# Performance work log

Hardware: AMD Instinct MI355X
Metric: run time of the kernel (lower is better)

## Reference

```python
import jax, jax.numpy as jnp
import numpy as np

N_EMB = 384
BLOCK = 128

def setup_inputs() -> dict:
    key = jax.random.key(0)
    k1, k2, k3, k4 = jax.random.split(key, 4)
    B, T, hs = 1024, 128, 64
    x = jax.random.normal(k1, (B, T, N_EMB), dtype=jnp.float32)
    Wk = jax.random.normal(k2, (hs, N_EMB), dtype=jnp.float32) * (N_EMB ** -0.5)
    Wq = jax.random.normal(k3, (hs, N_EMB), dtype=jnp.float32) * (N_EMB ** -0.5)
    Wv = jax.random.normal(k4, (hs, N_EMB), dtype=jnp.float32) * (N_EMB ** -0.5)
    return {"x": x, "Wk": Wk, "Wq": Wq, "Wv": Wv}

def reference(x, Wk, Wq, Wv):
    B, T, C = x.shape
    # nn.Linear(n_emb, head_size, bias=False): y = x @ W.T
    k = jnp.einsum('btc,hc->bth', x, Wk)  # [B,T,hs]
    q = jnp.einsum('btc,hc->bth', x, Wq)
    v = jnp.einsum('btc,hc->bth', x, Wv)
    # NOTE: source scales by C**-0.5 where C = n_emb (384), not head_size
    w = jnp.einsum('bth,bsh->bts', q, k) * (C ** -0.5)  # [B,T,T]
    causal = jnp.tril(jnp.ones((T, T), dtype=bool))
    w = jnp.where(causal, w, -jnp.inf)
    w = jax.nn.softmax(w, axis=-1)
    # dropout is identity in eval mode
    out = jnp.einsum('bts,bsh->bth', w, v)  # [B,T,hs]
    return out
```

## Files before the change

kernel.cpp:

```cpp
#include <hip/hip_runtime.h>

typedef __bf16 bf16_t;
typedef __attribute__((ext_vector_type(8))) __bf16 bf16x8;
typedef __attribute__((ext_vector_type(4))) float floatx4;

#define MFMA16(a, b, c) __builtin_amdgcn_mfma_f32_16x16x32_bf16((a), (b), (c), 0, 0, 0)

constexpr int TT = 128;
constexpr int CD = 384;
constexpr int HS = 64;
constexpr int W_ELEMS = HS * CD;

constexpr int QK_STR = 72;
constexpr int VT_STR = 136;
constexpr int QS_OFF = 0;
constexpr int KS_OFF = TT * QK_STR;
constexpr int VT_OFF = 2 * TT * QK_STR;
constexpr int PS_OFF = 0;
constexpr int SMEM_N = 2 * TT * QK_STR + HS * VT_STR;

__global__ void wconv_kernel(const float* __restrict__ wq, const float* __restrict__ wk,
                             const float* __restrict__ wv, bf16_t* __restrict__ out) {
    int i = blockIdx.x * 256 + threadIdx.x;
    if (i < W_ELEMS)            out[i] = (bf16_t)wq[i];
    else if (i < 2 * W_ELEMS)   out[i] = (bf16_t)wk[i - W_ELEMS];
    else if (i < 3 * W_ELEMS)   out[i] = (bf16_t)wv[i - 2 * W_ELEMS];
}

__launch_bounds__(256, 2)
__global__ void attn_kernel(const float* __restrict__ x, const bf16_t* __restrict__ wc,
                            float* __restrict__ out) {
    __shared__ bf16_t smem[SMEM_N];
    const int b    = blockIdx.x;
    const int lane = threadIdx.x & 63;
    const int w    = threadIdx.x >> 6;
    const int l15  = lane & 15;
    const int g    = lane >> 4;
    const float* xb = x + (size_t)b * TT * CD;

    floatx4 accq[2][4], acck[2][4], accv[2][4];
#pragma unroll
    for (int mt = 0; mt < 2; ++mt)
#pragma unroll
        for (int nt = 0; nt < 4; ++nt) {
            accq[mt][nt] = (floatx4)0.0f;
            acck[mt][nt] = (floatx4)0.0f;
            accv[mt][nt] = (floatx4)0.0f;
        }

    for (int kk = 0; kk < CD; kk += 32) {
        const int c = kk + 8 * g;
        bf16x8 a[2];
#pragma unroll
        for (int mt = 0; mt < 2; ++mt) {
            const int row = 32 * w + 16 * mt + l15;
            const float* p = xb + row * CD + c;
            float4 f0 = *(const float4*)p;
            float4 f1 = *(const float4*)(p + 4);
            bf16x8 t;
            t[0] = (bf16_t)f0.x; t[1] = (bf16_t)f0.y; t[2] = (bf16_t)f0.z; t[3] = (bf16_t)f0.w;
            t[4] = (bf16_t)f1.x; t[5] = (bf16_t)f1.y; t[6] = (bf16_t)f1.z; t[7] = (bf16_t)f1.w;
            a[mt] = t;
        }
#pragma unroll
        for (int nt = 0; nt < 4; ++nt) {
            const int h = 16 * nt + l15;
            bf16x8 bq = *(const bf16x8*)(wc + 0 * W_ELEMS + h * CD + c);
            bf16x8 bk = *(const bf16x8*)(wc + 1 * W_ELEMS + h * CD + c);
            bf16x8 bv = *(const bf16x8*)(wc + 2 * W_ELEMS + h * CD + c);
            accq[0][nt] = MFMA16(a[0], bq, accq[0][nt]);
            accq[1][nt] = MFMA16(a[1], bq, accq[1][nt]);
            acck[0][nt] = MFMA16(a[0], bk, acck[0][nt]);
            acck[1][nt] = MFMA16(a[1], bk, acck[1][nt]);
            accv[0][nt] = MFMA16(a[0], bv, accv[0][nt]);
            accv[1][nt] = MFMA16(a[1], bv, accv[1][nt]);
        }
    }

#pragma unroll
    for (int mt = 0; mt < 2; ++mt)
#pragma unroll
        for (int nt = 0; nt < 4; ++nt) {
            const int t0 = 32 * w + 16 * mt + 4 * g;
            const int h  = 16 * nt + l15;
#pragma unroll
            for (int r = 0; r < 4; ++r) {
                smem[QS_OFF + (t0 + r) * QK_STR + h] = (bf16_t)accq[mt][nt][r];
                smem[KS_OFF + (t0 + r) * QK_STR + h] = (bf16_t)acck[mt][nt][r];
                smem[VT_OFF + h * VT_STR + t0 + r]   = (bf16_t)accv[mt][nt][r];
            }
        }
    __syncthreads();

    floatx4 sacc[2][8];
#pragma unroll
    for (int mt = 0; mt < 2; ++mt)
#pragma unroll
        for (int nt = 0; nt < 8; ++nt) sacc[mt][nt] = (floatx4)0.0f;

#pragma unroll
    for (int kt = 0; kt < 2; ++kt) {
        const int hh = 32 * kt + 8 * g;
        bf16x8 aq[2];
        aq[0] = *(const bf16x8*)(smem + QS_OFF + (32 * w + l15) * QK_STR + hh);
        aq[1] = *(const bf16x8*)(smem + QS_OFF + (32 * w + 16 + l15) * QK_STR + hh);
#pragma unroll
        for (int nt = 0; nt < 8; ++nt) {
            if (16 * nt <= 32 * w + 31) {
                bf16x8 bk = *(const bf16x8*)(smem + KS_OFF + (16 * nt + l15) * QK_STR + hh);
                if (16 * nt <= 32 * w + 15) sacc[0][nt] = MFMA16(aq[0], bk, sacc[0][nt]);
                sacc[1][nt] = MFMA16(aq[1], bk, sacc[1][nt]);
            }
        }
    }
    __syncthreads();

    const float scale = 0.05103103630798287f;
#pragma unroll
    for (int mt = 0; mt < 2; ++mt) {
#pragma unroll
        for (int r = 0; r < 4; ++r) {
            const int t = 32 * w + 16 * mt + 4 * g + r;
            float vals[8];
            float vmax = -__builtin_inff();
#pragma unroll
            for (int nt = 0; nt < 8; ++nt) {
                const int s = 16 * nt + l15;
                float v = (s <= t) ? sacc[mt][nt][r] * scale : -__builtin_inff();
                vals[nt] = v;
                vmax = fmaxf(vmax, v);
            }
            vmax = fmaxf(vmax, __shfl_xor(vmax, 1));
            vmax = fmaxf(vmax, __shfl_xor(vmax, 2));
            vmax = fmaxf(vmax, __shfl_xor(vmax, 4));
            vmax = fmaxf(vmax, __shfl_xor(vmax, 8));
            float sum = 0.0f;
#pragma unroll
            for (int nt = 0; nt < 8; ++nt) {
                float e = __expf(vals[nt] - vmax);
                vals[nt] = e;
                sum += e;
            }
            sum += __shfl_xor(sum, 1);
            sum += __shfl_xor(sum, 2);
            sum += __shfl_xor(sum, 4);
            sum += __shfl_xor(sum, 8);
            const float inv = 1.0f / sum;
#pragma unroll
            for (int nt = 0; nt < 8; ++nt)
                smem[PS_OFF + t * VT_STR + 16 * nt + l15] = (bf16_t)(vals[nt] * inv);
        }
    }

    floatx4 oacc[2][4];
#pragma unroll
    for (int mt = 0; mt < 2; ++mt)
#pragma unroll
        for (int nt = 0; nt < 4; ++nt) oacc[mt][nt] = (floatx4)0.0f;

    for (int st = 0; st <= w; ++st) {
        const int ss = 32 * st + 8 * g;
        bf16x8 ap[2];
        ap[0] = *(const bf16x8*)(smem + PS_OFF + (32 * w + l15) * VT_STR + ss);
        ap[1] = *(const bf16x8*)(smem + PS_OFF + (32 * w + 16 + l15) * VT_STR + ss);
#pragma unroll
        for (int nt = 0; nt < 4; ++nt) {
            bf16x8 bv = *(const bf16x8*)(smem + VT_OFF + (16 * nt + l15) * VT_STR + ss);
            oacc[0][nt] = MFMA16(ap[0], bv, oacc[0][nt]);
            oacc[1][nt] = MFMA16(ap[1], bv, oacc[1][nt]);
        }
    }

    float* ob = out + (size_t)b * TT * HS;
#pragma unroll
    for (int mt = 0; mt < 2; ++mt)
#pragma unroll
        for (int nt = 0; nt < 4; ++nt) {
            const int t0 = 32 * w + 16 * mt + 4 * g;
            const int h  = 16 * nt + l15;
#pragma unroll
            for (int r = 0; r < 4; ++r)
                ob[(t0 + r) * HS + h] = oacc[mt][nt][r];
        }
}

extern "C" void kernel_launch(void* const* d_in, const int* in_sizes, int n_in,
                              void* d_out, int out_size, void* d_ws, size_t ws_size,
                              hipStream_t stream) {
    const float* x  = (const float*)d_in[0];
    const float* wk = (const float*)d_in[1];
    const float* wq = (const float*)d_in[2];
    const float* wv = (const float*)d_in[3];
    bf16_t* wc = (bf16_t*)d_ws;
    float* out = (float*)d_out;

    wconv_kernel<<<(3 * W_ELEMS + 255) / 256, 256, 0, stream>>>(wq, wk, wv, wc);
    attn_kernel<<<1024, 256, 0, stream>>>(x, wc, out);
}
```

Before: 342.2 us.

## Split fused attention into separate QKV projection and attention kernels via global workspace

```diff
diff --git a/kernel.cpp b/kernel.cpp
--- a/kernel.cpp
+++ b/kernel.cpp
@@ -1,6 +1,7 @@
 #include <hip/hip_runtime.h>
 
 typedef __bf16 bf16_t;
+typedef __attribute__((ext_vector_type(4))) __bf16 bf16x4;
 typedef __attribute__((ext_vector_type(8))) __bf16 bf16x8;
 typedef __attribute__((ext_vector_type(4))) float floatx4;
 
@@ -9,15 +10,10 @@
 constexpr int TT = 128;
 constexpr int CD = 384;
 constexpr int HS = 64;
+constexpr int BB = 1024;
 constexpr int W_ELEMS = HS * CD;
-
-constexpr int QK_STR = 72;
-constexpr int VT_STR = 136;
-constexpr int QS_OFF = 0;
-constexpr int KS_OFF = TT * QK_STR;
-constexpr int VT_OFF = 2 * TT * QK_STR;
-constexpr int PS_OFF = 0;
-constexpr int SMEM_N = 2 * TT * QK_STR + HS * VT_STR;
+constexpr size_t QKV_ELEMS = (size_t)BB * TT * HS;
+constexpr int PS_STR = 136;
 
 __global__ void wconv_kernel(const float* __restrict__ wq, const float* __restrict__ wk,
                              const float* __restrict__ wv, bf16_t* __restrict__ out) {
@@ -27,97 +23,94 @@
     else if (i < 3 * W_ELEMS)   out[i] = (bf16_t)wv[i - 2 * W_ELEMS];
 }
 
-__launch_bounds__(256, 2)
-__global__ void attn_kernel(const float* __restrict__ x, const bf16_t* __restrict__ wc,
-                            float* __restrict__ out) {
-    __shared__ bf16_t smem[SMEM_N];
-    const int b    = blockIdx.x;
+__launch_bounds__(256, 4)
+__global__ void qkv_kernel(const float* __restrict__ x, const bf16_t* __restrict__ wc,
+                           bf16_t* __restrict__ q, bf16_t* __restrict__ k,
+                           bf16_t* __restrict__ vt) {
     const int lane = threadIdx.x & 63;
     const int w    = threadIdx.x >> 6;
     const int l15  = lane & 15;
     const int g    = lane >> 4;
-    const float* xb = x + (size_t)b * TT * CD;
+    const int row0 = blockIdx.x * 64 + w * 16;
+    const float* xr = x + (size_t)(row0 + l15) * CD;
 
-    floatx4 accq[2][4], acck[2][4], accv[2][4];
+    floatx4 accq[4], acck[4], accv[4];
 #pragma unroll
-    for (int mt = 0; mt < 2; ++mt)
-#pragma unroll
-        for (int nt = 0; nt < 4; ++nt) {
-            accq[mt][nt] = (floatx4)0.0f;
-            acck[mt][nt] = (floatx4)0.0f;
-            accv[mt][nt] = (floatx4)0.0f;
-        }
+    for (int nt = 0; nt < 4; ++nt) {
+        accq[nt] = (floatx4)0.0f;
+        acck[nt] = (floatx4)0.0f;
+        accv[nt] = (floatx4)0.0f;
+    }
 
     for (int kk = 0; kk < CD; kk += 32) {
         const int c = kk + 8 * g;
-        bf16x8 a[2];
-#pragma unroll
-        for (int mt = 0; mt < 2; ++mt) {
-            const int row = 32 * w + 16 * mt + l15;
-            const float* p = xb + row * CD + c;
-            float4 f0 = *(const float4*)p;
-            float4 f1 = *(const float4*)(p + 4);
-            bf16x8 t;
-            t[0] = (bf16_t)f0.x; t[1] = (bf16_t)f0.y; t[2] = (bf16_t)f0.z; t[3] = (bf16_t)f0.w;
-            t[4] = (bf16_t)f1.x; t[5] = (bf16_t)f1.y; t[6] = (bf16_t)f1.z; t[7] = (bf16_t)f1.w;
-            a[mt] = t;
-        }
+        float4 f0 = *(const float4*)(xr + c);
+        float4 f1 = *(const float4*)(xr + c + 4);
+        bf16x8 a;
+        a[0] = (bf16_t)f0.x; a[1] = (bf16_t)f0.y; a[2] = (bf16_t)f0.z; a[3] = (bf16_t)f0.w;
+        a[4] = (bf16_t)f1.x; a[5] = (bf16_t)f1.y; a[6] = (bf16_t)f1.z; a[7] = (bf16_t)f1.w;
 #pragma unroll
         for (int nt = 0; nt < 4; ++nt) {
             const int h = 16 * nt + l15;
             bf16x8 bq = *(const bf16x8*)(wc + 0 * W_ELEMS + h * CD + c);
             bf16x8 bk = *(const bf16x8*)(wc + 1 * W_ELEMS + h * CD + c);
             bf16x8 bv = *(const bf16x8*)(wc + 2 * W_ELEMS + h * CD + c);
-            accq[0][nt] = MFMA16(a[0], bq, accq[0][nt]);
-            accq[1][nt] = MFMA16(a[1], bq, accq[1][nt]);
-            acck[0][nt] = MFMA16(a[0], bk, acck[0][nt]);
-            acck[1][nt] = MFMA16(a[1], bk, acck[1][nt]);
-            accv[0][nt] = MFMA16(a[0], bv, accv[0][nt]);
-            accv[1][nt] = MFMA16(a[1], bv, accv[1][nt]);
+            accq[nt] = MFMA16(a, bq, accq[nt]);
+            acck[nt] = MFMA16(a, bk, acck[nt]);
+            accv[nt] = MFMA16(a, bv, accv[nt]);
         }
     }
 
+    const int b  = row0 >> 7;
+    const int tl = (row0 & 127) + 4 * g;
+#pragma unroll
+    for (int nt = 0; nt < 4; ++nt) {
+        const int h = 16 * nt + l15;
+#pragma unroll
+        for (int r = 0; r < 4; ++r) {
+            const size_t rowg = (size_t)(row0 + 4 * g + r);
+            q[rowg * HS + h] = (bf16_t)accq[nt][r];
+            k[rowg * HS + h] = (bf16_t)acck[nt][r];
+        }
+        bf16x4 pv;
+        pv[0] = (bf16_t)accv[nt][0]; pv[1] = (bf16_t)accv[nt][1];
+        pv[2] = (bf16_t)accv[nt][2]; pv[3] = (bf16_t)accv[nt][3];
+        *(bf16x4*)(vt + (size_t)b * HS * TT + (size_t)h * TT + tl) = pv;
+    }
+}
+
+__launch_bounds__(256, 4)
+__global__ void attn2_kernel(const bf16_t* __restrict__ q, const bf16_t* __restrict__ k,
+                             const bf16_t* __restrict__ vt, float* __restrict__ out) {
+    __shared__ __align__(16) bf16_t pbuf[TT * PS_STR];
+    const int b    = blockIdx.x;
+    const int lane = threadIdx.x & 63;
+    const int w    = threadIdx.x >> 6;
+    const int l15  = lane & 15;
+    const int g    = lane >> 4;
+    const size_t qb = (size_t)b * TT * HS;
+    const float scale = 0.05103103630798287f;
+
+    bf16x8 aq[2][2];
 #pragma unroll
     for (int mt = 0; mt < 2; ++mt)
 #pragma unroll
-        for (int nt = 0; nt < 4; ++nt) {
-            const int t0 = 32 * w + 16 * mt + 4 * g;
-            const int h  = 16 * nt + l15;
+        for (int kt = 0; kt < 2; ++kt)
+            aq[mt][kt] = *(const bf16x8*)(q + qb + (size_t)(32 * w + 16 * mt + l15) * HS + 32 * kt + 8 * g);
+
 #pragma unroll
-            for (int r = 0; r < 4; ++r) {
-                smem[QS_OFF + (t0 + r) * QK_STR + h] = (bf16_t)accq[mt][nt][r];
-                smem[KS_OFF + (t0 + r) * QK_STR + h] = (bf16_t)acck[mt][nt][r];
-                smem[VT_OFF + h * VT_STR + t0 + r]   = (bf16_t)accv[mt][nt][r];
+    for (int mt = 0; mt < 2; ++mt) {
+        floatx4 sacc[8];
+#pragma unroll
+        for (int nt = 0; nt < 8; ++nt) sacc[nt] = (floatx4)0.0f;
+        const int ntmax = 2 * w + mt;
+#pragma unroll
+        for (int kt = 0; kt < 2; ++kt) {
+            for (int nt = 0; nt <= ntmax; ++nt) {
+                bf16x8 bk = *(const bf16x8*)(k + qb + (size_t)(16 * nt + l15) * HS + 32 * kt + 8 * g);
+                sacc[nt] = MFMA16(aq[mt][kt], bk, sacc[nt]);
             }
         }
-    __syncthreads();
-
-    floatx4 sacc[2][8];
-#pragma unroll
-    for (int mt = 0; mt < 2; ++mt)
-#pragma unroll
-        for (int nt = 0; nt < 8; ++nt) sacc[mt][nt] = (floatx4)0.0f;
-
-#pragma unroll
-    for (int kt = 0; kt < 2; ++kt) {
-        const int hh = 32 * kt + 8 * g;
-        bf16x8 aq[2];
-        aq[0] = *(const bf16x8*)(smem + QS_OFF + (32 * w + l15) * QK_STR + hh);
-        aq[1] = *(const bf16x8*)(smem + QS_OFF + (32 * w + 16 + l15) * QK_STR + hh);
-#pragma unroll
-        for (int nt = 0; nt < 8; ++nt) {
-            if (16 * nt <= 32 * w + 31) {
-                bf16x8 bk = *(const bf16x8*)(smem + KS_OFF + (16 * nt + l15) * QK_STR + hh);
-                if (16 * nt <= 32 * w + 15) sacc[0][nt] = MFMA16(aq[0], bk, sacc[0][nt]);
-                sacc[1][nt] = MFMA16(aq[1], bk, sacc[1][nt]);
-            }
-        }
-    }
-    __syncthreads();
-
-    const float scale = 0.05103103630798287f;
-#pragma unroll
-    for (int mt = 0; mt < 2; ++mt) {
 #pragma unroll
         for (int r = 0; r < 4; ++r) {
             const int t = 32 * w + 16 * mt + 4 * g + r;
@@ -126,7 +119,7 @@
 #pragma unroll
             for (int nt = 0; nt < 8; ++nt) {
                 const int s = 16 * nt + l15;
-                float v = (s <= t) ? sacc[mt][nt][r] * scale : -__builtin_inff();
+                float v = (nt <= ntmax && s <= t) ? sacc[nt][r] * scale : -__builtin_inff();
                 vals[nt] = v;
                 vmax = fmaxf(vmax, v);
             }
@@ -148,7 +141,7 @@
             const float inv = 1.0f / sum;
 #pragma unroll
             for (int nt = 0; nt < 8; ++nt)
-                smem[PS_OFF + t * VT_STR + 16 * nt + l15] = (bf16_t)(vals[nt] * inv);
+                pbuf[t * PS_STR + 16 * nt + l15] = (bf16_t)(vals[nt] * inv);
         }
     }
 
@@ -160,18 +153,17 @@
 
     for (int st = 0; st <= w; ++st) {
         const int ss = 32 * st + 8 * g;
-        bf16x8 ap[2];
-        ap[0] = *(const bf16x8*)(smem + PS_OFF + (32 * w + l15) * VT_STR + ss);
-        ap[1] = *(const bf16x8*)(smem + PS_OFF + (32 * w + 16 + l15) * VT_STR + ss);
+        bf16x8 ap0 = *(const bf16x8*)(pbuf + (32 * w + l15) * PS_STR + ss);
+        bf16x8 ap1 = *(const bf16x8*)(pbuf + (32 * w + 16 + l15) * PS_STR + ss);
 #pragma unroll
         for (int nt = 0; nt < 4; ++nt) {
-            bf16x8 bv = *(const bf16x8*)(smem + VT_OFF + (16 * nt + l15) * VT_STR + ss);
-            oacc[0][nt] = MFMA16(ap[0], bv, oacc[0][nt]);
-            oacc[1][nt] = MFMA16(ap[1], bv, oacc[1][nt]);
+            bf16x8 bv = *(const bf16x8*)(vt + (size_t)b * HS * TT + (size_t)(16 * nt + l15) * TT + ss);
+            oacc[0][nt] = MFMA16(ap0, bv, oacc[0][nt]);
+            oacc[1][nt] = MFMA16(ap1, bv, oacc[1][nt]);
         }
     }
 
-    float* ob = out + (size_t)b * TT * HS;
+    float* ob = out + qb;
 #pragma unroll
     for (int mt = 0; mt < 2; ++mt)
 #pragma unroll
@@ -180,7 +172,7 @@
             const int h  = 16 * nt + l15;
 #pragma unroll
             for (int r = 0; r < 4; ++r)
-                ob[(t0 + r) * HS + h] = oacc[mt][nt][r];
+                ob[(size_t)(t0 + r) * HS + h] = oacc[mt][nt][r];
         }
 }
 
@@ -191,9 +183,14 @@
     const float* wk = (const float*)d_in[1];
     const float* wq = (const float*)d_in[2];
     const float* wv = (const float*)d_in[3];
-    bf16_t* wc = (bf16_t*)d_ws;
     float* out = (float*)d_out;
 
+    bf16_t* wc = (bf16_t*)d_ws;
+    bf16_t* q  = wc + 3 * W_ELEMS;
+    bf16_t* k  = q + QKV_ELEMS;
+    bf16_t* vt = k + QKV_ELEMS;
+
     wconv_kernel<<<(3 * W_ELEMS + 255) / 256, 256, 0, stream>>>(wq, wk, wv, wc);
-    attn_kernel<<<1024, 256, 0, stream>>>(x, wc, out);
+    qkv_kernel<<<(BB * TT) / 64, 256, 0, stream>>>(x, wc, q, k, vt);
+    attn2_kernel<<<BB, 256, 0, stream>>>(q, k, vt, out);
 }
```

New measurement: 410.2 us. 1.2x slower.

## Pre-swizzle weights into MFMA fragment layout and double-buffer projection loads

Applied to the files above, without the earlier changes.

```diff
diff --git a/kernel.cpp b/kernel.cpp
--- a/kernel.cpp
+++ b/kernel.cpp
@@ -9,7 +9,7 @@
 constexpr int TT = 128;
 constexpr int CD = 384;
 constexpr int HS = 64;
-constexpr int W_ELEMS = HS * CD;
+constexpr int BB = 1024;
 
 constexpr int QK_STR = 72;
 constexpr int VT_STR = 136;
@@ -20,23 +20,35 @@
 constexpr int SMEM_N = 2 * TT * QK_STR + HS * VT_STR;
 
 __global__ void wconv_kernel(const float* __restrict__ wq, const float* __restrict__ wk,
-                             const float* __restrict__ wv, bf16_t* __restrict__ out) {
-    int i = blockIdx.x * 256 + threadIdx.x;
-    if (i < W_ELEMS)            out[i] = (bf16_t)wq[i];
-    else if (i < 2 * W_ELEMS)   out[i] = (bf16_t)wk[i - W_ELEMS];
-    else if (i < 3 * W_ELEMS)   out[i] = (bf16_t)wv[i - 2 * W_ELEMS];
+                             const float* __restrict__ wv, bf16_t* __restrict__ wf) {
+    const int t = blockIdx.x * 256 + threadIdx.x;
+    if (t >= 3 * 12 * 4 * 64) return;
+    const int lane = t & 63;
+    const int f    = t >> 6;
+    const int nt   = f & 3;
+    const int kki  = (f >> 2) % 12;
+    const int proj = f / 48;
+    const float* W = (proj == 0) ? wq : ((proj == 1) ? wk : wv);
+    const int h = 16 * nt + (lane & 15);
+    const int c = 32 * kki + 8 * (lane >> 4);
+    const float* src = W + h * CD + c;
+    bf16x8 o;
+#pragma unroll
+    for (int j = 0; j < 8; ++j) o[j] = (bf16_t)src[j];
+    *(bf16x8*)(wf + (size_t)t * 8) = o;
 }
 
 __launch_bounds__(256, 2)
-__global__ void attn_kernel(const float* __restrict__ x, const bf16_t* __restrict__ wc,
+__global__ void attn_kernel(const float* __restrict__ x, const bf16_t* __restrict__ wf,
                             float* __restrict__ out) {
-    __shared__ bf16_t smem[SMEM_N];
+    __shared__ __align__(16) bf16_t smem[SMEM_N];
     const int b    = blockIdx.x;
     const int lane = threadIdx.x & 63;
     const int w    = threadIdx.x >> 6;
     const int l15  = lane & 15;
     const int g    = lane >> 4;
     const float* xb = x + (size_t)b * TT * CD;
+    const bf16_t* wfl = wf + (size_t)lane * 8;
 
     floatx4 accq[2][4], acck[2][4], accv[2][4];
 #pragma unroll
@@ -48,32 +60,62 @@
             accv[mt][nt] = (floatx4)0.0f;
         }
 
-    for (int kk = 0; kk < CD; kk += 32) {
-        const int c = kk + 8 * g;
+    float4 xa0[2], xa1[2];
+    bf16x8 wb[12];
+#pragma unroll
+    for (int mt = 0; mt < 2; ++mt) {
+        const float* p = xb + (size_t)(32 * w + 16 * mt + l15) * CD + 8 * g;
+        xa0[mt] = *(const float4*)p;
+        xa1[mt] = *(const float4*)(p + 4);
+    }
+#pragma unroll
+    for (int pn = 0; pn < 12; ++pn) {
+        const int proj = pn >> 2, nt = pn & 3;
+        wb[pn] = *(const bf16x8*)(wfl + (size_t)((proj * 12 + 0) * 4 + nt) * 512);
+    }
+
+#pragma unroll
+    for (int kki = 0; kki < 12; ++kki) {
+        float4 xn0[2], xn1[2];
+        bf16x8 wn[12];
+        if (kki < 11) {
+            const int c = 32 * (kki + 1) + 8 * g;
+#pragma unroll
+            for (int mt = 0; mt < 2; ++mt) {
+                const float* p = xb + (size_t)(32 * w + 16 * mt + l15) * CD + c;
+                xn0[mt] = *(const float4*)p;
+                xn1[mt] = *(const float4*)(p + 4);
+            }
+#pragma unroll
+            for (int pn = 0; pn < 12; ++pn) {
+                const int proj = pn >> 2, nt = pn & 3;
+                wn[pn] = *(const bf16x8*)(wfl + (size_t)((proj * 12 + kki + 1) * 4 + nt) * 512);
+            }
+        }
         bf16x8 a[2];
 #pragma unroll
         for (int mt = 0; mt < 2; ++mt) {
-            const int row = 32 * w + 16 * mt + l15;
-            const float* p = xb + row * CD + c;
-            float4 f0 = *(const float4*)p;
-            float4 f1 = *(const float4*)(p + 4);
             bf16x8 t;
-            t[0] = (bf16_t)f0.x; t[1] = (bf16_t)f0.y; t[2] = (bf16_t)f0.z; t[3] = (bf16_t)f0.w;
-            t[4] = (bf16_t)f1.x; t[5] = (bf16_t)f1.y; t[6] = (bf16_t)f1.z; t[7] = (bf16_t)f1.w;
+            t[0] = (bf16_t)xa0[mt].x; t[1] = (bf16_t)xa0[mt].y;
+            t[2] = (bf16_t)xa0[mt].z; t[3] = (bf16_t)xa0[mt].w;
+            t[4] = (bf16_t)xa1[mt].x; t[5] = (bf16_t)xa1[mt].y;
+            t[6] = (bf16_t)xa1[mt].z; t[7] = (bf16_t)xa1[mt].w;
             a[mt] = t;
         }
 #pragma unroll
         for (int nt = 0; nt < 4; ++nt) {
-            const int h = 16 * nt + l15;
-            bf16x8 bq = *(const bf16x8*)(wc + 0 * W_ELEMS + h * CD + c);
-            bf16x8 bk = *(const bf16x8*)(wc + 1 * W_ELEMS + h * CD + c);
-            bf16x8 bv = *(const bf16x8*)(wc + 2 * W_ELEMS + h * CD + c);
-            accq[0][nt] = MFMA16(a[0], bq, accq[0][nt]);
-            accq[1][nt] = MFMA16(a[1], bq, accq[1][nt]);
-            acck[0][nt] = MFMA16(a[0], bk, acck[0][nt]);
-            acck[1][nt] = MFMA16(a[1], bk, acck[1][nt]);
-            accv[0][nt] = MFMA16(a[0], bv, accv[0][nt]);
-            accv[1][nt] = MFMA16(a[1], bv, accv[1][nt]);
+            accq[0][nt] = MFMA16(a[0], wb[0 + nt], accq[0][nt]);
+            accq[1][nt] = MFMA16(a[1], wb[0 + nt], accq[1][nt]);
+            acck[0][nt] = MFMA16(a[0], wb[4 + nt], acck[0][nt]);
+            acck[1][nt] = MFMA16(a[1], wb[4 + nt], acck[1][nt]);
+            accv[0][nt] = MFMA16(a[0], wb[8 + nt], accv[0][nt]);
+            accv[1][nt] = MFMA16(a[1], wb[8 + nt], accv[1][nt]);
+        }
+        if (kki < 11) {
+#pragma unroll
+            for (int mt = 0; mt < 2; ++mt) { xa0[mt] = xn0[mt]; xa1[mt] = xn1[mt]; }
+#pragma unroll
+            for (int pn = 0; pn < 12; ++pn) wb[pn] = wn[pn];
         }
     }
 
@@ -160,14 +202,13 @@
 
     for (int st = 0; st <= w; ++st) {
         const int ss = 32 * st + 8 * g;
-        bf16x8 ap[2];
-        ap[0] = *(const bf16x8*)(smem + PS_OFF + (32 * w + l15) * VT_STR + ss);
-        ap[1] = *(const bf16x8*)(smem + PS_OFF + (32 * w + 16 + l15) * VT_STR + ss);
+        bf16x8 ap0 = *(const bf16x8*)(smem + PS_OFF + (32 * w + l15) * VT_STR + ss);
+        bf16x8 ap1 = *(const bf16x8*)(smem + PS_OFF + (32 * w + 16 + l15) * VT_STR + ss);
 #pragma unroll
         for (int nt = 0; nt < 4; ++nt) {
             bf16x8 bv = *(const bf16x8*)(smem + VT_OFF + (16 * nt + l15) * VT_STR + ss);
-            oacc[0][nt] = MFMA16(ap[0], bv, oacc[0][nt]);
-            oacc[1][nt] = MFMA16(ap[1], bv, oacc[1][nt]);
+            oacc[0][nt] = MFMA16(ap0, bv, oacc[0][nt]);
+            oacc[1][nt] = MFMA16(ap1, bv, oacc[1][nt]);
         }
     }
 
@@ -180,7 +221,7 @@
             const int h  = 16 * nt + l15;
 #pragma unroll
             for (int r = 0; r < 4; ++r)
-                ob[(t0 + r) * HS + h] = oacc[mt][nt][r];
+                ob[(size_t)(t0 + r) * HS + h] = oacc[mt][nt][r];
         }
 }
 
@@ -191,9 +232,10 @@
     const float* wk = (const float*)d_in[1];
     const float* wq = (const float*)d_in[2];
     const float* wv = (const float*)d_in[3];
-    bf16_t* wc = (bf16_t*)d_ws;
     float* out = (float*)d_out;
 
-    wconv_kernel<<<(3 * W_ELEMS + 255) / 256, 256, 0, stream>>>(wq, wk, wv, wc);
-    attn_kernel<<<1024, 256, 0, stream>>>(x, wc, out);
+    bf16_t* wf = (bf16_t*)d_ws;
+
+    wconv_kernel<<<36, 256, 0, stream>>>(wq, wk, wv, wf);
+    attn_kernel<<<BB, 256, 0, stream>>>(x, wf, out);
 }
```

After: 329.2 us. 1.04x faster.
